# Kernel tuning notes

Hardware: AMD Instinct MI355X
Metric: run time of the kernel (lower is better)

## Reference

```python
import jax, jax.numpy as jnp
import numpy as np

NUM_HEADS = 16

def setup_inputs() -> dict:
    key = jax.random.key(0)
    k1, k2, k3 = jax.random.split(key, 3)
    B, T, C = 4, 2048, 2048
    x = jax.random.normal(k1, (B, T, C), dtype=jnp.float32)
    Wqkv = jax.random.normal(k2, (C, 3 * C), dtype=jnp.float32) * (C ** -0.5)
    bqkv = jnp.zeros((3 * C,), dtype=jnp.float32)
    Wproj = jax.random.normal(k3, (C, C), dtype=jnp.float32) * (C ** -0.5)
    bproj = jnp.zeros((C,), dtype=jnp.float32)
    return {"x": x, "Wqkv": Wqkv, "bqkv": bqkv, "Wproj": Wproj, "bproj": bproj}

def reference(x, Wqkv, bqkv, Wproj, bproj):
    B, T, C = x.shape
    H = NUM_HEADS
    D = C // H  # head_dim
    qkv = x @ Wqkv + bqkv                      # [B,T,3C]
    q, k, v = jnp.split(qkv, 3, axis=-1)
    # [B,T,C] -> [B,H,T,D]
    q = q.reshape(B, T, H, D).transpose(0, 2, 1, 3)
    k = k.reshape(B, T, H, D).transpose(0, 2, 1, 3)
    v = v.reshape(B, T, H, D).transpose(0, 2, 1, 3)
    scale = D ** -0.5
    scores = jnp.einsum('bhqd,bhkd->bhqk', q, k) * scale  # [B,H,T,T]
    causal = jnp.tril(jnp.ones((T, T), dtype=bool))
    scores = jnp.where(causal, scores, jnp.finfo(scores.dtype).min)
    attn = jax.nn.softmax(scores, axis=-1)
    out = jnp.einsum('bhqk,bhkd->bhqd', attn, v)           # [B,H,T,D]
    out = out.transpose(0, 2, 1, 3).reshape(B, T, C)
    return out @ Wproj + bproj
```

## Files before the change

### kernel.cpp

```cpp
#include <hip/hip_runtime.h>
#include <hip/hip_bf16.h>
#include <stdint.h>

typedef __attribute__((ext_vector_type(8))) short short8;
typedef __attribute__((ext_vector_type(4))) float f32x4;
typedef __attribute__((ext_vector_type(16))) float f32x16;
typedef __attribute__((ext_vector_type(2))) unsigned int uint2v;

__device__ __forceinline__ unsigned short f2bf(float f) {
  union { float f; unsigned int u; } v; v.f = f;
  unsigned int r = v.u + 0x7FFFu + ((v.u >> 16) & 1u);
  return (unsigned short)(r >> 16);
}

__device__ __forceinline__ unsigned int cvtpk(float lo, float hi) {
  unsigned int r;
  asm("v_cvt_pk_bf16_f32 %0, %1, %2" : "=v"(r) : "v"(lo), "v"(hi));
  return r;
}

#define GLOAD16(gsrc, ldst)                                                                  \
  __builtin_amdgcn_global_load_lds((const __attribute__((address_space(1))) void*)(gsrc),    \
                                   (__attribute__((address_space(3))) void*)(ldst), 16, 0, 0)

#define BAR() __builtin_amdgcn_s_barrier()
#define LGKMC(n) do { asm volatile("s_waitcnt lgkmcnt(" #n ")" ::: "memory"); \
                      __builtin_amdgcn_sched_barrier(0); } while (0)
#define LGKM0() LGKMC(0)
#define VMCNT0() asm volatile("s_waitcnt vmcnt(0)" ::: "memory")
#define VMCNT8() do { asm volatile("s_waitcnt vmcnt(8)" ::: "memory"); \
                      __builtin_amdgcn_sched_barrier(0); } while (0)
#define PRIO(x) __builtin_amdgcn_s_setprio(x)
#define MFMA16(d, a, b) d = __builtin_amdgcn_mfma_f32_16x16x32_bf16(a, b, d, 0, 0, 0)

__global__ __launch_bounds__(256) void cast_bf16_kernel(const float* __restrict__ in,
                                                        unsigned short* __restrict__ out) {
  int i = blockIdx.x * 256 + threadIdx.x;
  float4 v = ((const float4*)in)[i];
  ushort4 o;
  o.x = f2bf(v.x); o.y = f2bf(v.y); o.z = f2bf(v.z); o.w = f2bf(v.w);
  ((ushort4*)out)[i] = o;
}

__global__ __launch_bounds__(256) void transpose_cast_kernel(const float* __restrict__ W,
                                                             unsigned short* __restrict__ Wt,
                                                             int K, int N) {
  __shared__ float tile[32][33];
  int n0 = blockIdx.x * 32, k0 = blockIdx.y * 32;
  int tx = threadIdx.x, ty = threadIdx.y;
#pragma unroll
  for (int j = 0; j < 32; j += 8)
    tile[ty + j][tx] = W[(size_t)(k0 + ty + j) * N + n0 + tx];
  __syncthreads();
#pragma unroll
  for (int j = 0; j < 32; j += 8)
    Wt[(size_t)(n0 + ty + j) * K + k0 + tx] = f2bf(tile[tx][ty + j]);
}

__device__ __forceinline__ void stage_half(const unsigned short* __restrict__ gp, int K,
                                           int kt, int half, char* lds_mat, int tid) {
#pragma unroll
  for (int it = 0; it < 2; ++it) {
    int li = half * 1024 + it * 512 + tid;
    int r = li >> 3, c = li & 7;
    int cs = c ^ (r & 7);
    GLOAD16(gp + (size_t)r * K + kt * 64 + cs * 8, lds_mat + li * 16);
  }
}

__device__ __forceinline__ void gemm256_mainloop(const unsigned short* __restrict__ Ap,
                                                 const unsigned short* __restrict__ Bp,
                                                 int K, int tid, char* smem,
                                                 f32x4 acc[8][4]) {
  char* sa = smem;
  char* sb = smem + 65536;
  const int KT = K >> 6;

  int wid = tid >> 6, lane = tid & 63;
  int wr = wid >> 2, wc = wid & 3;
  int lg = lane >> 4, l15 = lane & 15;
  int swz7 = l15 & 7;

#define LDA(ab, m, kc) \
  (*(const short8*)((const unsigned short*)(ab) + (size_t)((wr * 128 + (m) * 16 + l15) * 64 + ((((kc) * 4 + lg) ^ swz7) * 8))))
#define LDB(bb, n, kc) \
  (*(const short8*)((const unsigned short*)(bb) + (size_t)((wc * 64 + (n) * 16 + l15) * 64 + ((((kc) * 4 + lg) ^ swz7) * 8))))

  stage_half(Bp, K, 0, 0, sb, tid);
  stage_half(Bp, K, 0, 1, sb, tid);
  stage_half(Ap, K, 0, 0, sa, tid);
  stage_half(Ap, K, 0, 1, sa, tid);
  stage_half(Bp, K, 1, 0, sb + 32768, tid);
  stage_half(Bp, K, 1, 1, sb + 32768, tid);
  stage_half(Ap, K, 1, 0, sa + 32768, tid);
  stage_half(Ap, K, 1, 1, sa + 32768, tid);
  VMCNT8();
  BAR();

  for (int t = 0; t < KT; ++t) {
    int p = t & 1;
    const char* ab = sa + p * 32768;
    const char* bb = sb + p * 32768;
    int kt2 = (t + 2 < KT) ? t + 2 : KT - 1;

    short8 bq01[2][2], bq23[2][2], aq[4][2], aq2[4][2];
#pragma unroll
    for (int n = 0; n < 2; ++n) { bq01[n][0] = LDB(bb, n, 0); bq01[n][1] = LDB(bb, n, 1); }
#pragma unroll
    for (int m = 0; m < 4; ++m) { aq[m][0] = LDA(ab, m, 0); aq[m][1] = LDA(ab, m, 1); }
#pragma unroll
    for (int n = 0; n < 2; ++n) { bq23[n][0] = LDB(bb, n + 2, 0); bq23[n][1] = LDB(bb, n + 2, 1); }
#pragma unroll
    for (int m = 0; m < 4; ++m) { aq2[m][0] = LDA(ab, m + 4, 0); aq2[m][1] = LDA(ab, m + 4, 1); }

    LGKMC(12);
    PRIO(1);
#pragma unroll
    for (int kc = 0; kc < 2; ++kc)
#pragma unroll
      for (int m = 0; m < 4; ++m)
#pragma unroll
        for (int n = 0; n < 2; ++n)
          MFMA16(acc[m][n], aq[m][kc], bq01[n][kc]);
    PRIO(0);

    LGKMC(8);
    BAR();
    stage_half(Bp, K, kt2, 0, sb + p * 32768, tid);
    stage_half(Bp, K, kt2, 1, sb + p * 32768, tid);

    PRIO(1);
#pragma unroll
    for (int kc = 0; kc < 2; ++kc)
#pragma unroll
      for (int m = 0; m < 4; ++m)
#pragma unroll
        for (int n = 0; n < 2; ++n)
          MFMA16(acc[m][n + 2], aq[m][kc], bq23[n][kc]);
    PRIO(0);

    LGKMC(0);
    PRIO(1);
#pragma unroll
    for (int kc = 0; kc < 2; ++kc)
#pragma unroll
      for (int m = 0; m < 4; ++m)
#pragma unroll
        for (int n = 0; n < 2; ++n)
          MFMA16(acc[m + 4][n + 2], aq2[m][kc], bq23[n][kc]);
    PRIO(0);

    BAR();
    stage_half(Ap, K, kt2, 0, sa + p * 32768, tid);
    stage_half(Ap, K, kt2, 1, sa + p * 32768, tid);
    PRIO(1);
#pragma unroll
    for (int kc = 0; kc < 2; ++kc)
#pragma unroll
      for (int m = 0; m < 4; ++m)
#pragma unroll
        for (int n = 0; n < 2; ++n)
          MFMA16(acc[m + 4][n], aq2[m][kc], bq01[n][kc]);
    PRIO(0);
    VMCNT8();
    BAR();
  }
#undef LDA
#undef LDB
}

__global__ __launch_bounds__(512, 2) void gemm_qkv256_kernel(const unsigned short* __restrict__ A,
                                                             const unsigned short* __restrict__ Bt,
                                                             const float* __restrict__ bias,
                                                             unsigned short* __restrict__ qb,
                                                             unsigned short* __restrict__ kb,
                                                             unsigned short* __restrict__ vtb) {
  extern __shared__ char smem[];
  int wg = blockIdx.x;
  int xcd = wg & 7, idx = wg >> 3;
  int bn = xcd * 3 + idx % 3;
  int bm = idx / 3;
  int tid = threadIdx.x;

  f32x4 acc[8][4];
  f32x4 zero = {0.f, 0.f, 0.f, 0.f};
#pragma unroll
  for (int m = 0; m < 8; ++m)
#pragma unroll
    for (int n = 0; n < 4; ++n) acc[m][n] = zero;

  gemm256_mainloop(A + (size_t)bm * 256 * 2048, Bt + (size_t)bn * 256 * 2048, 2048, tid, smem, acc);

  const float QSCALE = (float)(0.08838834764831845 * 1.4426950408889634);
  int wid = tid >> 6, lane = tid & 63;
  int wr = wid >> 2, wc = wid & 3, lg = lane >> 4, l15 = lane & 15;
  int l31 = lane & 31, hi = lane >> 5;

  if (bn >= 16) {
    VMCNT0();
    BAR();
#pragma unroll
    for (int n = 0; n < 4; ++n) {
      int cl = wc * 64 + n * 16 + l15;
      float bv = bias[bn * 256 + cl];
#pragma unroll
      for (int m = 0; m < 8; ++m) {
        int rl = wr * 128 + m * 16 + lg * 4;
        unsigned int w0 = cvtpk(acc[m][n][0] + bv, acc[m][n][1] + bv);
        unsigned int w1 = cvtpk(acc[m][n][2] + bv, acc[m][n][3] + bv);
        uint2v pk = {w0, w1};
        *(uint2v*)(smem + cl * 512 + ((rl * 2) ^ ((cl & 7) << 4))) = pk;
      }
    }
    LGKM0();
    BAR();
    int t0_abs = bm * 256;
    int bq_ = t0_abs >> 11, t0 = t0_abs & 2047;
    int h0 = (bn * 256 - 4096) >> 7;
#pragma unroll
    for (int i = 0; i < 16; ++i) {
      int dloc = i * 16 + wid * 2 + hi;
      short8 vrow = *(const short8*)(smem + dloc * 512 + ((l31 * 16) ^ ((dloc & 7) << 4)));
      int bh_ = bq_ * 16 + h0 + (dloc >> 7);
      int d = dloc & 127;
      *(short8*)(vtb + ((size_t)bh_ * 128 + d) * 2048 + t0 + l31 * 8) = vrow;
    }
  } else {
    VMCNT0();
    BAR();
    bool isq = (bn < 8);
#pragma unroll
    for (int n = 0; n < 4; ++n) {
      int cl = wc * 64 + n * 16 + l15;
      float bv = bias[bn * 256 + cl];
#pragma unroll
      for (int m = 0; m < 8; ++m) {
#pragma unroll
        for (int g = 0; g < 4; ++g) {
          int rl = wr * 128 + m * 16 + lg * 4 + g;
          float r = acc[m][n][g] + bv;
          if (isq) r *= QSCALE;
          *(unsigned short*)(smem + rl * 512 + ((cl * 2) ^ ((rl & 15) << 4))) = f2bf(r);
        }
      }
    }
    LGKM0();
    BAR();
    int t0_abs = bm * 256;
    unsigned short* dst = isq ? qb : kb;
    int h0 = ((bn & 7) * 256) >> 7;
#pragma unroll
    for (int i = 0; i < 16; ++i) {
      int id = i * 512 + tid;
      int rl = id >> 5, c8 = id & 31;
      short8 v = *(const short8*)(smem + rl * 512 + ((c8 * 16) ^ ((rl & 15) << 4)));
      int row = t0_abs + rl;
      int b = row >> 11, t = row & 2047;
      int h = h0 + (c8 >> 4);
      int d0 = (c8 & 15) * 8;
      *(short8*)(dst + ((size_t)(b * 16 + h) * 2048 + t) * 128 + d0) = v;
    }
  }
}

__global__ __launch_bounds__(512, 2) void gemm_proj256_kernel(const unsigned short* __restrict__ A,
                                                              const unsigned short* __restrict__ Bt,
                                                              const float* __restrict__ bias,
                                                              float* __restrict__ out) {
  extern __shared__ char smem[];
  int wg = blockIdx.x;
  int bm = wg >> 3, bn = wg & 7;
  int tid = threadIdx.x;

  f32x4 acc[8][4];
  f32x4 zero = {0.f, 0.f, 0.f, 0.f};
#pragma unroll
  for (int m = 0; m < 8; ++m)
#pragma unroll
    for (int n = 0; n < 4; ++n) acc[m][n] = zero;

  gemm256_mainloop(A + (size_t)bm * 256 * 2048, Bt + (size_t)bn * 256 * 2048, 2048, tid, smem, acc);

  int wid = tid >> 6, lane = tid & 63;
  int wr = wid >> 2, wc = wid & 3, lg = lane >> 4, l15 = lane & 15;
#pragma unroll
  for (int n = 0; n < 4; ++n) {
    int col = bn * 256 + wc * 64 + n * 16 + l15;
    float bv = bias[col];
#pragma unroll
    for (int m = 0; m < 8; ++m) {
#pragma unroll
      for (int g = 0; g < 4; ++g) {
        int row = bm * 256 + wr * 128 + m * 16 + lg * 4 + g;
        out[(size_t)row * 2048 + col] = acc[m][n][g] + bv;
      }
    }
  }
}

__global__ __launch_bounds__(512) void attn_kernel(const unsigned short* __restrict__ qb,
                                                   const unsigned short* __restrict__ kb,
                                                   const unsigned short* __restrict__ vtb,
                                                   unsigned short* __restrict__ ob) {
  extern __shared__ char asmem[];
  int bh = blockIdx.x;
  int pairi = blockIdx.y;
  int b = bh >> 4, h = bh & 15;
  int tid = threadIdx.x, wid = tid >> 6, lane = tid & 63;
  int l31 = lane & 31, hi = lane >> 5;

  const unsigned short* Q  = qb  + (size_t)bh * 2048 * 128;
  const unsigned short* K  = kb  + (size_t)bh * 2048 * 128;
  const unsigned short* Vt = vtb + (size_t)bh * 128 * 2048;

#pragma unroll 1
  for (int pass = 0; pass < 2; ++pass) {
    int qt = pass == 0 ? (7 - pairi) : pairi;
    int NT = 4 * qt + 4;
    int qbase = qt * 256 + wid * 32;
    int qrow = qbase + l31;

    short8 qf[8];
#pragma unroll
    for (int kc = 0; kc < 8; ++kc)
      qf[kc] = *(const short8*)(Q + (size_t)qrow * 128 + kc * 16 + hi * 8);

    f32x16 o0 = {}, o1 = {}, o2 = {}, o3 = {};
    float m_run = -1e30f, l_run = 0.f;

    {
      char* kb_ = asmem;
#pragma unroll
      for (int it = 0; it < 2; ++it) {
        int li = it * 512 + tid;
        int r = li >> 4, c = li & 15;
        GLOAD16(K + (size_t)r * 128 + (c ^ (r & 7)) * 8, kb_ + li * 16);
      }
#pragma unroll
      for (int it = 0; it < 2; ++it) {
        int li = it * 512 + tid;
        int r = li >> 3, c = li & 7;
        GLOAD16(Vt + (size_t)r * 2048 + (c ^ (r & 7)) * 8, kb_ + 16384 + li * 16);
      }
    }
    VMCNT0();
    BAR();

#pragma unroll 1
    for (int kt = 0; kt < NT; ++kt) {
      char* cb = asmem + ((kt & 1) << 15);
      if (kt + 1 < NT) {
        char* nb = asmem + (((kt + 1) & 1) << 15);
        int kt1 = kt + 1;
#pragma unroll
        for (int it = 0; it < 2; ++it) {
          int li = it * 512 + tid;
          int r = li >> 4, c = li & 15;
          GLOAD16(K + (size_t)(kt1 * 64 + r) * 128 + (c ^ (r & 7)) * 8, nb + li * 16);
        }
#pragma unroll
        for (int it = 0; it < 2; ++it) {
          int li = it * 512 + tid;
          int r = li >> 3, c = li & 7;
          GLOAD16(Vt + (size_t)r * 2048 + kt1 * 64 + (c ^ (r & 7)) * 8, nb + 16384 + li * 16);
        }
      }

      bool active = (kt * 64 <= qbase + 31);
      if (active) {
        const char* k_l = cb;
        const char* v_l = cb + 16384;

        f32x16 s0v = {}, s1v = {};
        PRIO(1);
#pragma unroll
        for (int kc = 0; kc < 8; ++kc) {
          int cg = kc * 2 + hi;
          int sw = l31 & 7;
          short8 kf0 = *(const short8*)(k_l + l31 * 256 + ((cg ^ sw) * 16));
          s0v = __builtin_amdgcn_mfma_f32_32x32x16_bf16(kf0, qf[kc], s0v, 0, 0, 0);
          short8 kf1 = *(const short8*)(k_l + (32 + l31) * 256 + ((cg ^ sw) * 16));
          s1v = __builtin_amdgcn_mfma_f32_32x32x16_bf16(kf1, qf[kc], s1v, 0, 0, 0);
        }
        PRIO(0);

        if (kt * 64 + 63 > qbase) {
          int kvb = kt * 64 + 4 * hi;
#pragma unroll
          for (int r = 0; r < 16; ++r) {
            int kv = kvb + (r & 3) + 8 * (r >> 2);
            if (kv > qrow) s0v[r] = -1e30f;
            if (kv + 32 > qrow) s1v[r] = -1e30f;
          }
        }

        float tmax[16];
#pragma unroll
        for (int i = 0; i < 16; ++i) tmax[i] = fmaxf(s0v[i], s1v[i]);
#pragma unroll
        for (int st = 8; st >= 1; st >>= 1)
#pragma unroll
          for (int i = 0; i < st; ++i) tmax[i] = fmaxf(tmax[i], tmax[i + st]);
        float pmax = fmaxf(tmax[0], __shfl_xor(tmax[0], 32));

        if (!__all(pmax <= m_run + 8.0f)) {
          float mn = fmaxf(m_run, pmax);
          float alpha = exp2f(m_run - mn);
          m_run = mn; l_run *= alpha;
          o0 *= alpha; o1 *= alpha; o2 *= alpha; o3 *= alpha;
        }

#pragma unroll
        for (int i = 0; i < 16; ++i) {
          s0v[i] = exp2f(s0v[i] - m_run);
          s1v[i] = exp2f(s1v[i] - m_run);
        }
        float tsum[16];
#pragma unroll
        for (int i = 0; i < 16; ++i) tsum[i] = s0v[i] + s1v[i];
#pragma unroll
        for (int st = 8; st >= 1; st >>= 1)
#pragma unroll
          for (int i = 0; i < st; ++i) tsum[i] += tsum[i + st];
        float rsum = tsum[0] + __shfl_xor(tsum[0], 32);
        l_run += rsum;

#define BUILD_PA(sv, base, out)                                                \
        {                                                                      \
          unsigned int a_ = cvtpk(sv[base + 0], sv[base + 1]);                 \
          unsigned int c_ = cvtpk(sv[base + 2], sv[base + 3]);                 \
          unsigned int b_ = cvtpk(sv[base + 4], sv[base + 5]);                 \
          unsigned int d_ = cvtpk(sv[base + 6], sv[base + 7]);                 \
          uint2v r0_ = __builtin_amdgcn_permlane32_swap(a_, b_, false, false); \
          uint2v r1_ = __builtin_amdgcn_permlane32_swap(c_, d_, false, false); \
          union { unsigned int u[4]; short8 v; } uu_;                          \
          uu_.u[0] = r0_[0]; uu_.u[1] = r1_[0]; uu_.u[2] = r0_[1]; uu_.u[3] = r1_[1]; \
          out = uu_.v;                                                         \
        }
        short8 pa0, pa1, pa2, pa3;
        BUILD_PA(s0v, 0, pa0);
        BUILD_PA(s0v, 8, pa1);
        BUILD_PA(s1v, 0, pa2);
        BUILD_PA(s1v, 8, pa3);
#undef BUILD_PA

        PRIO(1);
#define PV_STEP(ovar, dt)                                                          \
        {                                                                          \
          int rv_ = dt * 32 + l31;                                                 \
          const char* vb_ = v_l + rv_ * 128;                                       \
          int sw_ = rv_ & 7;                                                       \
          short8 v0_ = *(const short8*)(vb_ + (((0 + hi) ^ sw_) * 16));            \
          ovar = __builtin_amdgcn_mfma_f32_32x32x16_bf16(v0_, pa0, ovar, 0, 0, 0); \
          short8 v1_ = *(const short8*)(vb_ + (((2 + hi) ^ sw_) * 16));            \
          ovar = __builtin_amdgcn_mfma_f32_32x32x16_bf16(v1_, pa1, ovar, 0, 0, 0); \
          short8 v2_ = *(const short8*)(vb_ + (((4 + hi) ^ sw_) * 16));            \
          ovar = __builtin_amdgcn_mfma_f32_32x32x16_bf16(v2_, pa2, ovar, 0, 0, 0); \
          short8 v3_ = *(const short8*)(vb_ + (((6 + hi) ^ sw_) * 16));            \
          ovar = __builtin_amdgcn_mfma_f32_32x32x16_bf16(v3_, pa3, ovar, 0, 0, 0); \
        }
        PV_STEP(o0, 0)
        PV_STEP(o1, 1)
        PV_STEP(o2, 2)
        PV_STEP(o3, 3)
#undef PV_STEP
        PRIO(0);
      }

      VMCNT0();
      BAR();
    }

    float inv = 1.0f / l_run;
    size_t orow = (size_t)(b * 2048 + qt * 256 + wid * 32 + l31);
    unsigned short* ob_p = ob + orow * 2048 + h * 128;
#define STORE_DT(ovar, dt)                                                         \
    {                                                                              \
      _Pragma("unroll")                                                            \
      for (int rq = 0; rq < 4; ++rq) {                                             \
        unsigned int w0 = cvtpk(ovar[rq * 4 + 0] * inv, ovar[rq * 4 + 1] * inv);   \
        unsigned int w1 = cvtpk(ovar[rq * 4 + 2] * inv, ovar[rq * 4 + 3] * inv);   \
        uint2v st = {w0, w1};                                                      \
        *(uint2v*)(ob_p + dt * 32 + rq * 8 + 4 * hi) = st;                         \
      }                                                                            \
    }
    STORE_DT(o0, 0)
    STORE_DT(o1, 1)
    STORE_DT(o2, 2)
    STORE_DT(o3, 3)
#undef STORE_DT
  }
}

extern "C" void kernel_launch(void* const* d_in, const int* in_sizes, int n_in,
                              void* d_out, int out_size, void* d_ws, size_t ws_size,
                              hipStream_t stream) {
  const float* x     = (const float*)d_in[0];
  const float* Wqkv  = (const float*)d_in[1];
  const float* bqkv  = (const float*)d_in[2];
  const float* Wproj = (const float*)d_in[3];
  const float* bproj = (const float*)d_in[4];
  float* out = (float*)d_out;

  char* ws = (char*)d_ws;
  unsigned short* x_bf   = (unsigned short*)ws;
  unsigned short* wqkvt  = (unsigned short*)(ws + 33554432);
  unsigned short* wprojt = (unsigned short*)(ws + 33554432 + 25165824);
  unsigned short* qb     = (unsigned short*)(ws + 67108864);
  unsigned short* kb     = (unsigned short*)(ws + 100663296);
  unsigned short* vtb    = (unsigned short*)(ws + 134217728);

  (void)hipFuncSetAttribute((const void*)gemm_qkv256_kernel,
                            hipFuncAttributeMaxDynamicSharedMemorySize, 131072);
  (void)hipFuncSetAttribute((const void*)gemm_proj256_kernel,
                            hipFuncAttributeMaxDynamicSharedMemorySize, 131072);
  (void)hipFuncSetAttribute((const void*)attn_kernel,
                            hipFuncAttributeMaxDynamicSharedMemorySize, 65536);

  cast_bf16_kernel<<<16384, 256, 0, stream>>>(x, x_bf);
  transpose_cast_kernel<<<dim3(192, 64), dim3(32, 8), 0, stream>>>(Wqkv, wqkvt, 2048, 6144);
  transpose_cast_kernel<<<dim3(64, 64), dim3(32, 8), 0, stream>>>(Wproj, wprojt, 2048, 2048);
  gemm_qkv256_kernel<<<768, 512, 131072, stream>>>(x_bf, wqkvt, bqkv, qb, kb, vtb);
  attn_kernel<<<dim3(64, 4), 512, 65536, stream>>>(qb, kb, vtb, x_bf );
  gemm_proj256_kernel<<<256, 512, 131072, stream>>>(x_bf, wprojt, bproj, out);
}
```

Baseline: 393.5 us.

## Shrink GEMM tiles to 128x256 with single-buffered LDS and 4 waves

Both GEMM kernels drop from 256x256 tiles with 8 waves and a double-buffered, prefetch-two-ahead pipeline to 128x256 tiles with 4 waves and a single LDS buffer. The loop now loads, waits fully on vmcnt(0), and computes without overlapping global loads and MFMA work. Grids double and LDS per block halves, which raises block count and occupancy at the cost of losing load/compute overlap and reusing A less per block. The epilogues are remapped to the new wave layout.

Measured after the change: 397.7 us. About the same (+1.1%).

```diff
diff --git a/kernel.cpp b/kernel.cpp
--- a/kernel.cpp
+++ b/kernel.cpp
@@ -24,12 +24,9 @@
                                    (__attribute__((address_space(3))) void*)(ldst), 16, 0, 0)
 
 #define BAR() __builtin_amdgcn_s_barrier()
-#define LGKMC(n) do { asm volatile("s_waitcnt lgkmcnt(" #n ")" ::: "memory"); \
-                      __builtin_amdgcn_sched_barrier(0); } while (0)
-#define LGKM0() LGKMC(0)
+#define LGKM0() do { asm volatile("s_waitcnt lgkmcnt(0)" ::: "memory"); \
+                     __builtin_amdgcn_sched_barrier(0); } while (0)
 #define VMCNT0() asm volatile("s_waitcnt vmcnt(0)" ::: "memory")
-#define VMCNT8() do { asm volatile("s_waitcnt vmcnt(8)" ::: "memory"); \
-                      __builtin_amdgcn_sched_barrier(0); } while (0)
 #define PRIO(x) __builtin_amdgcn_s_setprio(x)
 #define MFMA16(d, a, b) d = __builtin_amdgcn_mfma_f32_16x16x32_bf16(a, b, d, 0, 0, 0)
 
@@ -57,119 +54,89 @@
     Wt[(size_t)(n0 + ty + j) * K + k0 + tx] = f2bf(tile[tx][ty + j]);
 }
 
-__device__ __forceinline__ void stage_half(const unsigned short* __restrict__ gp, int K,
-                                           int kt, int half, char* lds_mat, int tid) {
-#pragma unroll
-  for (int it = 0; it < 2; ++it) {
-    int li = half * 1024 + it * 512 + tid;
+__device__ __forceinline__ void stageA128(const unsigned short* __restrict__ gp, int K,
+                                          int kt, char* lds, int tid) {
+#pragma unroll
+  for (int it = 0; it < 4; ++it) {
+    int li = it * 256 + tid;
     int r = li >> 3, c = li & 7;
-    int cs = c ^ (r & 7);
-    GLOAD16(gp + (size_t)r * K + kt * 64 + cs * 8, lds_mat + li * 16);
-  }
-}
-
-__device__ __forceinline__ void gemm256_mainloop(const unsigned short* __restrict__ Ap,
-                                                 const unsigned short* __restrict__ Bp,
-                                                 int K, int tid, char* smem,
-                                                 f32x4 acc[8][4]) {
+    GLOAD16(gp + (size_t)r * K + kt * 64 + (c ^ (r & 7)) * 8, lds + li * 16);
+  }
+}
+__device__ __forceinline__ void stageB256(const unsigned short* __restrict__ gp, int K,
+                                          int kt, char* lds, int tid) {
+#pragma unroll
+  for (int it = 0; it < 8; ++it) {
+    int li = it * 256 + tid;
+    int r = li >> 3, c = li & 7;
+    GLOAD16(gp + (size_t)r * K + kt * 64 + (c ^ (r & 7)) * 8, lds + li * 16);
+  }
+}
+
+__device__ __forceinline__ void gemm128x256_mainloop(const unsigned short* __restrict__ Ap,
+                                                     const unsigned short* __restrict__ Bp,
+                                                     int K, int tid, char* smem,
+                                                     f32x4 acc[4][8]) {
   char* sa = smem;
-  char* sb = smem + 65536;
+  char* sb = smem + 16384;
   const int KT = K >> 6;
 
   int wid = tid >> 6, lane = tid & 63;
-  int wr = wid >> 2, wc = wid & 3;
+  int wr = wid >> 1, wc = wid & 1;
   int lg = lane >> 4, l15 = lane & 15;
   int swz7 = l15 & 7;
 
-#define LDA(ab, m, kc) \
-  (*(const short8*)((const unsigned short*)(ab) + (size_t)((wr * 128 + (m) * 16 + l15) * 64 + ((((kc) * 4 + lg) ^ swz7) * 8))))
-#define LDB(bb, n, kc) \
-  (*(const short8*)((const unsigned short*)(bb) + (size_t)((wc * 64 + (n) * 16 + l15) * 64 + ((((kc) * 4 + lg) ^ swz7) * 8))))
-
-  stage_half(Bp, K, 0, 0, sb, tid);
-  stage_half(Bp, K, 0, 1, sb, tid);
-  stage_half(Ap, K, 0, 0, sa, tid);
-  stage_half(Ap, K, 0, 1, sa, tid);
-  stage_half(Bp, K, 1, 0, sb + 32768, tid);
-  stage_half(Bp, K, 1, 1, sb + 32768, tid);
-  stage_half(Ap, K, 1, 0, sa + 32768, tid);
-  stage_half(Ap, K, 1, 1, sa + 32768, tid);
-  VMCNT8();
+#define LDA(m, kc) \
+  (*(const short8*)((const unsigned short*)sa + (size_t)((wr * 64 + (m) * 16 + l15) * 64 + ((((kc) * 4 + lg) ^ swz7) * 8))))
+#define LDB(n, kc) \
+  (*(const short8*)((const unsigned short*)sb + (size_t)((wc * 128 + (n) * 16 + l15) * 64 + ((((kc) * 4 + lg) ^ swz7) * 8))))
+
+  stageA128(Ap, K, 0, sa, tid);
+  stageB256(Bp, K, 0, sb, tid);
+  VMCNT0();
   BAR();
 
   for (int t = 0; t < KT; ++t) {
-    int p = t & 1;
-    const char* ab = sa + p * 32768;
-    const char* bb = sb + p * 32768;
-    int kt2 = (t + 2 < KT) ? t + 2 : KT - 1;
-
-    short8 bq01[2][2], bq23[2][2], aq[4][2], aq2[4][2];
-#pragma unroll
-    for (int n = 0; n < 2; ++n) { bq01[n][0] = LDB(bb, n, 0); bq01[n][1] = LDB(bb, n, 1); }
-#pragma unroll
-    for (int m = 0; m < 4; ++m) { aq[m][0] = LDA(ab, m, 0); aq[m][1] = LDA(ab, m, 1); }
-#pragma unroll
-    for (int n = 0; n < 2; ++n) { bq23[n][0] = LDB(bb, n + 2, 0); bq23[n][1] = LDB(bb, n + 2, 1); }
-#pragma unroll
-    for (int m = 0; m < 4; ++m) { aq2[m][0] = LDA(ab, m + 4, 0); aq2[m][1] = LDA(ab, m + 4, 1); }
-
-    LGKMC(12);
+    short8 aq[4][2], bq[4][2];
+#pragma unroll
+    for (int m = 0; m < 4; ++m) { aq[m][0] = LDA(m, 0); aq[m][1] = LDA(m, 1); }
+#pragma unroll
+    for (int n = 0; n < 4; ++n) { bq[n][0] = LDB(n, 0); bq[n][1] = LDB(n, 1); }
+    LGKM0();
     PRIO(1);
 #pragma unroll
     for (int kc = 0; kc < 2; ++kc)
 #pragma unroll
       for (int m = 0; m < 4; ++m)
 #pragma unroll
-        for (int n = 0; n < 2; ++n)
-          MFMA16(acc[m][n], aq[m][kc], bq01[n][kc]);
+        for (int n = 0; n < 4; ++n)
+          MFMA16(acc[m][n], aq[m][kc], bq[n][kc]);
     PRIO(0);
-
-    LGKMC(8);
+#pragma unroll
+    for (int n = 0; n < 4; ++n) { bq[n][0] = LDB(n + 4, 0); bq[n][1] = LDB(n + 4, 1); }
+    LGKM0();
+    PRIO(1);
+#pragma unroll
+    for (int kc = 0; kc < 2; ++kc)
+#pragma unroll
+      for (int m = 0; m < 4; ++m)
+#pragma unroll
+        for (int n = 0; n < 4; ++n)
+          MFMA16(acc[m][n + 4], aq[m][kc], bq[n][kc]);
+    PRIO(0);
     BAR();
-    stage_half(Bp, K, kt2, 0, sb + p * 32768, tid);
-    stage_half(Bp, K, kt2, 1, sb + p * 32768, tid);
-
-    PRIO(1);
-#pragma unroll
-    for (int kc = 0; kc < 2; ++kc)
-#pragma unroll
-      for (int m = 0; m < 4; ++m)
-#pragma unroll
-        for (int n = 0; n < 2; ++n)
-          MFMA16(acc[m][n + 2], aq[m][kc], bq23[n][kc]);
-    PRIO(0);
-
-    LGKMC(0);
-    PRIO(1);
-#pragma unroll
-    for (int kc = 0; kc < 2; ++kc)
-#pragma unroll
-      for (int m = 0; m < 4; ++m)
-#pragma unroll
-        for (int n = 0; n < 2; ++n)
-          MFMA16(acc[m + 4][n + 2], aq2[m][kc], bq23[n][kc]);
-    PRIO(0);
-
-    BAR();
-    stage_half(Ap, K, kt2, 0, sa + p * 32768, tid);
-    stage_half(Ap, K, kt2, 1, sa + p * 32768, tid);
-    PRIO(1);
-#pragma unroll
-    for (int kc = 0; kc < 2; ++kc)
-#pragma unroll
-      for (int m = 0; m < 4; ++m)
-#pragma unroll
-        for (int n = 0; n < 2; ++n)
-          MFMA16(acc[m + 4][n], aq2[m][kc], bq01[n][kc]);
-    PRIO(0);
-    VMCNT8();
+    if (t + 1 < KT) {
+      stageA128(Ap, K, t + 1, sa, tid);
+      stageB256(Bp, K, t + 1, sb, tid);
+      VMCNT0();
+    }
     BAR();
   }
 #undef LDA
 #undef LDB
 }
 
-__global__ __launch_bounds__(512, 2) void gemm_qkv256_kernel(const unsigned short* __restrict__ A,
+__global__ __launch_bounds__(256, 2) void gemm_qkv256_kernel(const unsigned short* __restrict__ A,
                                                              const unsigned short* __restrict__ Bt,
                                                              const float* __restrict__ bias,
                                                              unsigned short* __restrict__ qb,
@@ -182,62 +149,57 @@
   int bm = idx / 3;
   int tid = threadIdx.x;
 
-  f32x4 acc[8][4];
+  f32x4 acc[4][8];
   f32x4 zero = {0.f, 0.f, 0.f, 0.f};
 #pragma unroll
-  for (int m = 0; m < 8; ++m)
-#pragma unroll
-    for (int n = 0; n < 4; ++n) acc[m][n] = zero;
-
-  gemm256_mainloop(A + (size_t)bm * 256 * 2048, Bt + (size_t)bn * 256 * 2048, 2048, tid, smem, acc);
+  for (int m = 0; m < 4; ++m)
+#pragma unroll
+    for (int n = 0; n < 8; ++n) acc[m][n] = zero;
+
+  gemm128x256_mainloop(A + (size_t)bm * 128 * 2048, Bt + (size_t)bn * 256 * 2048, 2048, tid, smem, acc);
 
   const float QSCALE = (float)(0.08838834764831845 * 1.4426950408889634);
   int wid = tid >> 6, lane = tid & 63;
-  int wr = wid >> 2, wc = wid & 3, lg = lane >> 4, l15 = lane & 15;
-  int l31 = lane & 31, hi = lane >> 5;
+  int wr = wid >> 1, wc = wid & 1, lg = lane >> 4, l15 = lane & 15;
 
   if (bn >= 16) {
-    VMCNT0();
-    BAR();
-#pragma unroll
-    for (int n = 0; n < 4; ++n) {
-      int cl = wc * 64 + n * 16 + l15;
+    int h0v = (bn - 16) * 2;
+#pragma unroll
+    for (int n = 0; n < 8; ++n) {
+      int cl = wc * 128 + n * 16 + l15;
       float bv = bias[bn * 256 + cl];
 #pragma unroll
-      for (int m = 0; m < 8; ++m) {
-        int rl = wr * 128 + m * 16 + lg * 4;
+      for (int m = 0; m < 4; ++m) {
+        int rl = wr * 64 + m * 16 + lg * 4;
         unsigned int w0 = cvtpk(acc[m][n][0] + bv, acc[m][n][1] + bv);
         unsigned int w1 = cvtpk(acc[m][n][2] + bv, acc[m][n][3] + bv);
         uint2v pk = {w0, w1};
-        *(uint2v*)(smem + cl * 512 + ((rl * 2) ^ ((cl & 7) << 4))) = pk;
+        *(uint2v*)(smem + cl * 256 + ((rl * 2) ^ ((cl & 7) << 4))) = pk;
       }
     }
     LGKM0();
     BAR();
-    int t0_abs = bm * 256;
-    int bq_ = t0_abs >> 11, t0 = t0_abs & 2047;
-    int h0 = (bn * 256 - 4096) >> 7;
+    int b = (bm * 128) >> 11, t0 = (bm * 128) & 2047;
 #pragma unroll
     for (int i = 0; i < 16; ++i) {
-      int dloc = i * 16 + wid * 2 + hi;
-      short8 vrow = *(const short8*)(smem + dloc * 512 + ((l31 * 16) ^ ((dloc & 7) << 4)));
-      int bh_ = bq_ * 16 + h0 + (dloc >> 7);
+      int id = i * 256 + tid;
+      int dloc = id >> 4, c = id & 15;
+      short8 v = *(const short8*)(smem + dloc * 256 + ((c * 16) ^ ((dloc & 7) << 4)));
+      int bh_ = b * 16 + h0v + (dloc >> 7);
       int d = dloc & 127;
-      *(short8*)(vtb + ((size_t)bh_ * 128 + d) * 2048 + t0 + l31 * 8) = vrow;
+      *(short8*)(vtb + ((size_t)bh_ * 128 + d) * 2048 + t0 + c * 8) = v;
     }
   } else {
-    VMCNT0();
-    BAR();
     bool isq = (bn < 8);
 #pragma unroll
-    for (int n = 0; n < 4; ++n) {
-      int cl = wc * 64 + n * 16 + l15;
+    for (int n = 0; n < 8; ++n) {
+      int cl = wc * 128 + n * 16 + l15;
       float bv = bias[bn * 256 + cl];
 #pragma unroll
-      for (int m = 0; m < 8; ++m) {
+      for (int m = 0; m < 4; ++m) {
 #pragma unroll
         for (int g = 0; g < 4; ++g) {
-          int rl = wr * 128 + m * 16 + lg * 4 + g;
+          int rl = wr * 64 + m * 16 + lg * 4 + g;
           float r = acc[m][n][g] + bv;
           if (isq) r *= QSCALE;
           *(unsigned short*)(smem + rl * 512 + ((cl * 2) ^ ((rl & 15) << 4))) = f2bf(r);
@@ -246,15 +208,14 @@
     }
     LGKM0();
     BAR();
-    int t0_abs = bm * 256;
     unsigned short* dst = isq ? qb : kb;
-    int h0 = ((bn & 7) * 256) >> 7;
+    int h0 = (bn & 7) * 2;
 #pragma unroll
     for (int i = 0; i < 16; ++i) {
-      int id = i * 512 + tid;
+      int id = i * 256 + tid;
       int rl = id >> 5, c8 = id & 31;
       short8 v = *(const short8*)(smem + rl * 512 + ((c8 * 16) ^ ((rl & 15) << 4)));
-      int row = t0_abs + rl;
+      int row = bm * 128 + rl;
       int b = row >> 11, t = row & 2047;
       int h = h0 + (c8 >> 4);
       int d0 = (c8 & 15) * 8;
@@ -263,7 +224,7 @@
   }
 }
 
-__global__ __launch_bounds__(512, 2) void gemm_proj256_kernel(const unsigned short* __restrict__ A,
+__global__ __launch_bounds__(256, 2) void gemm_proj256_kernel(const unsigned short* __restrict__ A,
                                                               const unsigned short* __restrict__ Bt,
                                                               const float* __restrict__ bias,
                                                               float* __restrict__ out) {
@@ -272,26 +233,26 @@
   int bm = wg >> 3, bn = wg & 7;
   int tid = threadIdx.x;
 
-  f32x4 acc[8][4];
+  f32x4 acc[4][8];
   f32x4 zero = {0.f, 0.f, 0.f, 0.f};
 #pragma unroll
-  for (int m = 0; m < 8; ++m)
-#pragma unroll
-    for (int n = 0; n < 4; ++n) acc[m][n] = zero;
-
-  gemm256_mainloop(A + (size_t)bm * 256 * 2048, Bt + (size_t)bn * 256 * 2048, 2048, tid, smem, acc);
+  for (int m = 0; m < 4; ++m)
+#pragma unroll
+    for (int n = 0; n < 8; ++n) acc[m][n] = zero;
+
+  gemm128x256_mainloop(A + (size_t)bm * 128 * 2048, Bt + (size_t)bn * 256 * 2048, 2048, tid, smem, acc);
 
   int wid = tid >> 6, lane = tid & 63;
-  int wr = wid >> 2, wc = wid & 3, lg = lane >> 4, l15 = lane & 15;
-#pragma unroll
-  for (int n = 0; n < 4; ++n) {
-    int col = bn * 256 + wc * 64 + n * 16 + l15;
+  int wr = wid >> 1, wc = wid & 1, lg = lane >> 4, l15 = lane & 15;
+#pragma unroll
+  for (int n = 0; n < 8; ++n) {
+    int col = bn * 256 + wc * 128 + n * 16 + l15;
     float bv = bias[col];
 #pragma unroll
-    for (int m = 0; m < 8; ++m) {
+    for (int m = 0; m < 4; ++m) {
 #pragma unroll
       for (int g = 0; g < 4; ++g) {
-        int row = bm * 256 + wr * 128 + m * 16 + lg * 4 + g;
+        int row = bm * 128 + wr * 64 + m * 16 + lg * 4 + g;
         out[(size_t)row * 2048 + col] = acc[m][n][g] + bv;
       }
     }
@@ -511,16 +472,16 @@
   unsigned short* vtb    = (unsigned short*)(ws + 134217728);
 
   (void)hipFuncSetAttribute((const void*)gemm_qkv256_kernel,
-                            hipFuncAttributeMaxDynamicSharedMemorySize, 131072);
+                            hipFuncAttributeMaxDynamicSharedMemorySize, 65536);
   (void)hipFuncSetAttribute((const void*)gemm_proj256_kernel,
-                            hipFuncAttributeMaxDynamicSharedMemorySize, 131072);
+                            hipFuncAttributeMaxDynamicSharedMemorySize, 65536);
   (void)hipFuncSetAttribute((const void*)attn_kernel,
                             hipFuncAttributeMaxDynamicSharedMemorySize, 65536);
 
   cast_bf16_kernel<<<16384, 256, 0, stream>>>(x, x_bf);
   transpose_cast_kernel<<<dim3(192, 64), dim3(32, 8), 0, stream>>>(Wqkv, wqkvt, 2048, 6144);
   transpose_cast_kernel<<<dim3(64, 64), dim3(32, 8), 0, stream>>>(Wproj, wprojt, 2048, 2048);
-  gemm_qkv256_kernel<<<768, 512, 131072, stream>>>(x_bf, wqkvt, bqkv, qb, kb, vtb);
+  gemm_qkv256_kernel<<<1536, 256, 65536, stream>>>(x_bf, wqkvt, bqkv, qb, kb, vtb);
   attn_kernel<<<dim3(64, 4), 512, 65536, stream>>>(qb, kb, vtb, x_bf );
-  gemm_proj256_kernel<<<256, 512, 131072, stream>>>(x_bf, wprojt, bproj, out);
-}
+  gemm_proj256_kernel<<<512, 256, 65536, stream>>>(x_bf, wprojt, bproj, out);
+}
```
